# Optimization experiments

Hardware: AMD Instinct MI355X
Metric: run time of the kernel (lower is better)

The kernel has to match this reference:

```python
import jax, jax.numpy as jnp
import numpy as np

T = 10            # inference steps (PCLayer.T)
LOCAL_LR = 0.001  # local_learning_rate
CLAMP = 1.0       # PCLayer.clamp_value


def setup_inputs() -> dict:
    key = jax.random.key(0)
    k1, k2 = jax.random.split(key)
    B, S, H_out, H_in = 8, 1024, 3072, 768
    target_activity = jax.random.normal(k1, (B, S, H_out), dtype=jnp.float32)
    # nn.Linear(H_in, H_out) weight: [H_out, H_in]
    W = jax.random.normal(k2, (H_out, H_in), dtype=jnp.float32) * (1.0 / np.sqrt(H_in))
    b = jnp.zeros((H_out,), dtype=jnp.float32)
    return {"target_activity": target_activity, "W": W, "b": b}


def reference(target_activity, W, b):
    # PCLayer forward, layer_type='fc1' (linear): T-step energy-gradient
    # fixed-point inference on latent x of shape [B, S, H_in].
    B, S, _ = target_activity.shape
    H_in = W.shape[1]
    x0 = jnp.zeros((B, S, H_in), dtype=target_activity.dtype)  # x_init

    def step(x, _):
        mu = jnp.einsum('bsi,oi->bso', x, W) + b       # prediction [B,S,H_out]
        err = target_activity - mu                      # prediction error
        # x <- x - lr * dE/dx, E = 0.5*||err||^2  =>  dE/dx = -err @ W
        x = x + LOCAL_LR * jnp.einsum('bso,oi->bsi', err, W)
        x = jnp.clip(x, -CLAMP, CLAMP)
        return x, None

    x, _ = jax.lax.scan(step, x0, None, length=T)
    return x
```

## Files before the change

kernel.cpp:

```cpp
#include <hip/hip_runtime.h>
#include <stdint.h>


typedef short bf16x8 __attribute__((ext_vector_type(8)));
typedef float f32x4  __attribute__((ext_vector_type(4)));
typedef unsigned short u16;
typedef unsigned int uint_as1 __attribute__((address_space(1)));
typedef unsigned int uint_as3 __attribute__((address_space(3)));

__device__ __forceinline__ u16 f2bf(float f) {
  union { float f; unsigned int i; } x; x.f = f;
  unsigned int r = x.i + 0x7fffu + ((x.i >> 16) & 1u);
  return (u16)(r >> 16);
}
__device__ __forceinline__ void gl2lds16(const void* g, void* l) {
  __builtin_amdgcn_global_load_lds((uint_as1*)(uintptr_t)g,
                                   (uint_as3*)(uintptr_t)l, 16, 0, 0);
}

template<int TM, int NK, int EPI>
__global__ __launch_bounds__(256, 2)
void gemm_lds(const u16* __restrict__ A, const u16* __restrict__ B,
              float* __restrict__ Cf, u16* __restrict__ Cb,
              float alpha, int K, int ldc, int kc, long zstride)
{
  constexpr int FM  = TM / 32;
  constexpr int RPW = TM / 4;
  __shared__ u16 As[TM * 32 * NK];
  __shared__ u16 Bs[128 * 32 * NK];
  const int tid = threadIdx.x, w = tid >> 6, lane = tid & 63;
  const int lm = lane & 15, quad = lane >> 4;
  const int wm = w & 1, wn = w >> 1;
  const int m0 = blockIdx.x * TM, n0 = blockIdx.y * 128;
  const long k0 = (long)blockIdx.z * kc;
  const int r = lane >> 2, q = lane & 3;
  const u16* Ag = A + (long)(m0 + w * RPW + r) * K + k0 + q * 8;
  const u16* Bg = B + (long)(n0 + w * 32 + r) * K + k0 + q * 8;
  u16* Asl = As + w * RPW * 32;
  u16* Bsl = Bs + w * 1024;

  f32x4 acc[FM][4] = {};

  for (int kk = 0; kk < kc; kk += 32 * NK) {
#pragma unroll
    for (int h = 0; h < NK; ++h) {
#pragma unroll
      for (int l = 0; l < RPW / 16; ++l)
        gl2lds16(Ag + (long)(l * 16) * K + kk + h * 32,
                 Asl + h * TM * 32 + l * 512);
      gl2lds16(Bg + kk + h * 32, Bsl + h * 4096);
      gl2lds16(Bg + 16 * (long)K + kk + h * 32, Bsl + h * 4096 + 512);
    }
    __syncthreads();
#pragma unroll
    for (int h = 0; h < NK; ++h) {
      bf16x8 af[FM], bv[4];
#pragma unroll
      for (int i = 0; i < FM; ++i)
        af[i] = *(const bf16x8*)(As + h * TM * 32 +
                                 (wm * (TM / 2) + i * 16 + lm) * 32 + quad * 8);
#pragma unroll
      for (int j = 0; j < 4; ++j)
        bv[j] = *(const bf16x8*)(Bs + h * 4096 +
                                 (wn * 64 + j * 16 + lm) * 32 + quad * 8);
#pragma unroll
      for (int i = 0; i < FM; ++i)
#pragma unroll
        for (int j = 0; j < 4; ++j)
          acc[i][j] = __builtin_amdgcn_mfma_f32_16x16x32_bf16(af[i], bv[j],
                                                              acc[i][j], 0, 0, 0);
    }
    __syncthreads();
  }

  const int rbase = m0 + wm * (TM / 2) + quad * 4;
  const int cbase = n0 + wn * 64 + lm;
  const long zoff = (long)blockIdx.z * zstride;
#pragma unroll
  for (int i = 0; i < FM; ++i)
#pragma unroll
    for (int j = 0; j < 4; ++j) {
      const int col = cbase + j * 16;
#pragma unroll
      for (int rr = 0; rr < 4; ++rr) {
        const long idx = (long)(rbase + i * 16 + rr) * ldc + col;
        const float v = alpha * acc[i][j][rr];
        if constexpr (EPI == 0) Cf[zoff + idx] = v;
        else                    Cb[idx] = f2bf(v);
      }
    }
}

__global__ void conv_all(const float* __restrict__ t, const float* __restrict__ bias,
                         const float* __restrict__ W, u16* __restrict__ tb,
                         u16* __restrict__ Wb, u16* __restrict__ WTb)
{
  const int bx = blockIdx.x, tid = threadIdx.x;
  if (bx < 24576) {
    const long i4 = (long)bx * 256 + tid;
    const float4 v = ((const float4*)t)[i4];
    const float4 bb = ((const float4*)bias)[(int)(i4 % 768)];
    ushort4 o;
    o.x = f2bf(v.x - bb.x); o.y = f2bf(v.y - bb.y);
    o.z = f2bf(v.z - bb.z); o.w = f2bf(v.w - bb.w);
    ((ushort4*)tb)[i4] = o;
  } else {
    const int i4 = (bx - 24576) * 256 + tid;
    const float4 v = ((const float4*)W)[i4];
    ushort4 o;
    o.x = f2bf(v.x); o.y = f2bf(v.y); o.z = f2bf(v.z); o.w = f2bf(v.w);
    ((ushort4*)Wb)[i4] = o;
    const int rr = i4 / 192, c = (i4 - rr * 192) * 4;
    WTb[(long)(c + 0) * 3072 + rr] = o.x;
    WTb[(long)(c + 1) * 3072 + rr] = o.y;
    WTb[(long)(c + 2) * 3072 + rr] = o.z;
    WTb[(long)(c + 3) * 3072 + rr] = o.w;
  }
}

__global__ void red_e(const float* __restrict__ Ep, float* __restrict__ Ef,
                      u16* __restrict__ Eb)
{
  const int i4 = blockIdx.x * 256 + threadIdx.x;
  float4 s = make_float4(0.f, 0.f, 0.f, 0.f);
#pragma unroll
  for (int z = 0; z < 4; ++z) {
    const float4 p = ((const float4*)Ep)[(long)z * 147456 + i4];
    s.x += p.x; s.y += p.y; s.z += p.z; s.w += p.w;
  }
  ((float4*)Ef)[i4] = s;
  ushort4 o; o.x = f2bf(s.x); o.y = f2bf(s.y); o.z = f2bf(s.z); o.w = f2bf(s.w);
  ((ushort4*)Eb)[i4] = o;
}

__global__ void red_m(const float* __restrict__ P2p, const float* __restrict__ Ef,
                      u16* __restrict__ Mb, float lr)
{
  const int i4 = blockIdx.x * 256 + threadIdx.x;
  float4 s = make_float4(0.f, 0.f, 0.f, 0.f);
#pragma unroll
  for (int z = 0; z < 4; ++z) {
    const float4 p = ((const float4*)P2p)[(long)z * 147456 + i4];
    s.x += p.x; s.y += p.y; s.z += p.z; s.w += p.w;
  }
  const float4 e = ((const float4*)Ef)[i4];
  const int rr = i4 / 192, c = (i4 - rr * 192) * 4;
  float4 m;
  m.x = lr * (-45.f * e.x + 120.f * s.x) + (rr == c + 0 ? 0.01f : 0.f);
  m.y = lr * (-45.f * e.y + 120.f * s.y) + (rr == c + 1 ? 0.01f : 0.f);
  m.z = lr * (-45.f * e.z + 120.f * s.z) + (rr == c + 2 ? 0.01f : 0.f);
  m.w = lr * (-45.f * e.w + 120.f * s.w) + (rr == c + 3 ? 0.01f : 0.f);
  ushort4 o; o.x = f2bf(m.x); o.y = f2bf(m.y); o.z = f2bf(m.z); o.w = f2bf(m.w);
  ((ushort4*)Mb)[i4] = o;
}

extern "C" void kernel_launch(void* const* d_in, const int* in_sizes, int n_in,
                              void* d_out, int out_size, void* d_ws, size_t ws_size,
                              hipStream_t stream)
{
  const float* t    = (const float*)d_in[0];
  const float* W    = (const float*)d_in[1];
  const float* bias = (const float*)d_in[2];
  float* out = (float*)d_out;

  char* p = (char*)d_ws;
  u16*   tb  = (u16*)(p + 0);
  u16*   Wb  = (u16*)(p + 50331648);
  u16*   WTb = (u16*)(p + 55050240);
  u16*   Apb = (u16*)(p + 59768832);
  u16*   Eb  = (u16*)(p + 64487424);
  u16*   Mb  = (u16*)(p + 65667072);
  float* Ef  = (float*)(p + 66846720);
  float* R   = (float*)(p + 69206016);
  const float lr = 0.001f;

  conv_all<<<26880, 256, 0, stream>>>(t, bias, W, tb, Wb, WTb);
  gemm_lds<64, 2, 0><<<dim3(12, 6, 4), 256, 0, stream>>>(
      WTb, WTb, R, nullptr, lr, 3072, 768, 768, 589824);
  red_e<<<576, 256, 0, stream>>>(R, Ef, Eb);
  gemm_lds<64, 2, 0><<<dim3(12, 6, 4), 256, 0, stream>>>(
      Eb, Eb, R, nullptr, 1.f, 768, 768, 192, 589824);
  red_m<<<576, 256, 0, stream>>>(R, Ef, Mb, lr);
  gemm_lds<64, 2, 1><<<dim3(12, 24, 1), 256, 0, stream>>>(
      Mb, Wb, nullptr, Apb, 1.f, 768, 3072, 768, 0);
  gemm_lds<128, 2, 0><<<dim3(64, 6, 1), 256, 0, stream>>>(
      tb, Apb, out, nullptr, 1.f, 3072, 768, 3072, 0);
}
```

Before: 276.4 us.

## Reassociate final product through t·W and transpose W via LDS tiles

New measurement: 270.7 us. -2.1%, faster.

```diff
diff --git a/kernel.cpp b/kernel.cpp
--- a/kernel.cpp
+++ b/kernel.cpp
@@ -8,6 +8,9 @@
 typedef unsigned int uint_as1 __attribute__((address_space(1)));
 typedef unsigned int uint_as3 __attribute__((address_space(3)));
 
+__device__ __forceinline__ float bf2f(u16 u) {
+  union { unsigned int i; float f; } x; x.i = ((unsigned int)u) << 16; return x.f;
+}
 __device__ __forceinline__ u16 f2bf(float f) {
   union { float f; unsigned int i; } x; x.f = f;
   unsigned int r = x.i + 0x7fffu + ((x.i >> 16) & 1u);
@@ -22,7 +25,8 @@
 __global__ __launch_bounds__(256, 2)
 void gemm_lds(const u16* __restrict__ A, const u16* __restrict__ B,
               float* __restrict__ Cf, u16* __restrict__ Cb,
-              float alpha, int K, int ldc, int kc, long zstride)
+              const u16* __restrict__ Yb, float alpha, float beta,
+              int K, int ldc, int kc, long zstride)
 {
   constexpr int FM  = TM / 32;
   constexpr int RPW = TM / 4;
@@ -85,16 +89,18 @@
       for (int rr = 0; rr < 4; ++rr) {
         const long idx = (long)(rbase + i * 16 + rr) * ldc + col;
         const float v = alpha * acc[i][j][rr];
-        if constexpr (EPI == 0) Cf[zoff + idx] = v;
-        else                    Cb[idx] = f2bf(v);
+        if constexpr (EPI == 0)      Cf[zoff + idx] = v;
+        else if constexpr (EPI == 1) Cb[idx] = f2bf(v);
+        else                         Cf[idx] = v + beta * bf2f(Yb[idx]);
       }
     }
 }
 
 __global__ void conv_all(const float* __restrict__ t, const float* __restrict__ bias,
                          const float* __restrict__ W, u16* __restrict__ tb,
-                         u16* __restrict__ Wb, u16* __restrict__ WTb)
-{
+                         u16* __restrict__ WTb)
+{
+  __shared__ u16 lds[64 * 72];
   const int bx = blockIdx.x, tid = threadIdx.x;
   if (bx < 24576) {
     const long i4 = (long)bx * 256 + tid;
@@ -105,27 +111,37 @@
     o.z = f2bf(v.z - bb.z); o.w = f2bf(v.w - bb.w);
     ((ushort4*)tb)[i4] = o;
   } else {
-    const int i4 = (bx - 24576) * 256 + tid;
-    const float4 v = ((const float4*)W)[i4];
-    ushort4 o;
-    o.x = f2bf(v.x); o.y = f2bf(v.y); o.z = f2bf(v.z); o.w = f2bf(v.w);
-    ((ushort4*)Wb)[i4] = o;
-    const int rr = i4 / 192, c = (i4 - rr * 192) * 4;
-    WTb[(long)(c + 0) * 3072 + rr] = o.x;
-    WTb[(long)(c + 1) * 3072 + rr] = o.y;
-    WTb[(long)(c + 2) * 3072 + rr] = o.z;
-    WTb[(long)(c + 3) * 3072 + rr] = o.w;
-  }
-}
-
-__global__ void red_e(const float* __restrict__ Ep, float* __restrict__ Ef,
+    const int bt = bx - 24576;
+    const int o0 = (bt / 12) * 64, i0 = (bt % 12) * 64;
+    const int ol = tid >> 2, cg = tid & 3;
+#pragma unroll
+    for (int p = 0; p < 4; ++p) {
+      const float4 v = *(const float4*)(W + (long)(o0 + ol) * 768 + i0 + (cg + p * 4) * 4);
+      const int ib = (cg + p * 4) * 4;
+      lds[(ib + 0) * 72 + ol] = f2bf(v.x);
+      lds[(ib + 1) * 72 + ol] = f2bf(v.y);
+      lds[(ib + 2) * 72 + ol] = f2bf(v.z);
+      lds[(ib + 3) * 72 + ol] = f2bf(v.w);
+    }
+    __syncthreads();
+    const int cl = tid >> 2, og = tid & 3;
+    const u16* src = lds + cl * 72 + og * 16;
+    u16* dst = WTb + (long)(i0 + cl) * 3072 + o0 + og * 16;
+    ((ushort4*)dst)[0] = ((const ushort4*)src)[0];
+    ((ushort4*)dst)[1] = ((const ushort4*)src)[1];
+    ((ushort4*)dst)[2] = ((const ushort4*)src)[2];
+    ((ushort4*)dst)[3] = ((const ushort4*)src)[3];
+  }
+}
+
+__global__ void red_e(const float* __restrict__ R, float* __restrict__ Ef,
                       u16* __restrict__ Eb)
 {
   const int i4 = blockIdx.x * 256 + threadIdx.x;
   float4 s = make_float4(0.f, 0.f, 0.f, 0.f);
 #pragma unroll
-  for (int z = 0; z < 4; ++z) {
-    const float4 p = ((const float4*)Ep)[(long)z * 147456 + i4];
+  for (int z = 0; z < 6; ++z) {
+    const float4 p = ((const float4*)R)[(long)z * 147456 + i4];
     s.x += p.x; s.y += p.y; s.z += p.z; s.w += p.w;
   }
   ((float4*)Ef)[i4] = s;
@@ -133,25 +149,23 @@
   ((ushort4*)Eb)[i4] = o;
 }
 
-__global__ void red_m(const float* __restrict__ P2p, const float* __restrict__ Ef,
-                      u16* __restrict__ Mb, float lr)
+__global__ void red_s(const float* __restrict__ R, const float* __restrict__ Ef,
+                      u16* __restrict__ Spb)
 {
   const int i4 = blockIdx.x * 256 + threadIdx.x;
   float4 s = make_float4(0.f, 0.f, 0.f, 0.f);
 #pragma unroll
-  for (int z = 0; z < 4; ++z) {
-    const float4 p = ((const float4*)P2p)[(long)z * 147456 + i4];
+  for (int z = 0; z < 6; ++z) {
+    const float4 p = ((const float4*)R)[(long)z * 147456 + i4];
     s.x += p.x; s.y += p.y; s.z += p.z; s.w += p.w;
   }
   const float4 e = ((const float4*)Ef)[i4];
-  const int rr = i4 / 192, c = (i4 - rr * 192) * 4;
-  float4 m;
-  m.x = lr * (-45.f * e.x + 120.f * s.x) + (rr == c + 0 ? 0.01f : 0.f);
-  m.y = lr * (-45.f * e.y + 120.f * s.y) + (rr == c + 1 ? 0.01f : 0.f);
-  m.z = lr * (-45.f * e.z + 120.f * s.z) + (rr == c + 2 ? 0.01f : 0.f);
-  m.w = lr * (-45.f * e.w + 120.f * s.w) + (rr == c + 3 ? 0.01f : 0.f);
-  ushort4 o; o.x = f2bf(m.x); o.y = f2bf(m.y); o.z = f2bf(m.z); o.w = f2bf(m.w);
-  ((ushort4*)Mb)[i4] = o;
+  ushort4 o;
+  o.x = f2bf(-45.f * e.x + 120.f * s.x);
+  o.y = f2bf(-45.f * e.y + 120.f * s.y);
+  o.z = f2bf(-45.f * e.z + 120.f * s.z);
+  o.w = f2bf(-45.f * e.w + 120.f * s.w);
+  ((ushort4*)Spb)[i4] = o;
 }
 
 extern "C" void kernel_launch(void* const* d_in, const int* in_sizes, int n_in,
@@ -165,24 +179,23 @@
 
   char* p = (char*)d_ws;
   u16*   tb  = (u16*)(p + 0);
-  u16*   Wb  = (u16*)(p + 50331648);
-  u16*   WTb = (u16*)(p + 55050240);
-  u16*   Apb = (u16*)(p + 59768832);
-  u16*   Eb  = (u16*)(p + 64487424);
-  u16*   Mb  = (u16*)(p + 65667072);
-  float* Ef  = (float*)(p + 66846720);
-  float* R   = (float*)(p + 69206016);
+  u16*   WTb = (u16*)(p + 50331648);
+  float* Ef  = (float*)(p + 55050240);
+  u16*   Eb  = (u16*)(p + 57409536);
+  u16*   Spb = (u16*)(p + 58589184);
+  float* R   = (float*)(p + 59768832);
+  u16*   yb  = (u16*)(p + 59768832);
   const float lr = 0.001f;
 
-  conv_all<<<26880, 256, 0, stream>>>(t, bias, W, tb, Wb, WTb);
-  gemm_lds<64, 2, 0><<<dim3(12, 6, 4), 256, 0, stream>>>(
-      WTb, WTb, R, nullptr, lr, 3072, 768, 768, 589824);
+  conv_all<<<25152, 256, 0, stream>>>(t, bias, W, tb, WTb);
+  gemm_lds<64, 2, 0><<<dim3(12, 6, 6), 256, 0, stream>>>(
+      WTb, WTb, R, nullptr, nullptr, lr, 0.f, 3072, 768, 512, 589824);
   red_e<<<576, 256, 0, stream>>>(R, Ef, Eb);
-  gemm_lds<64, 2, 0><<<dim3(12, 6, 4), 256, 0, stream>>>(
-      Eb, Eb, R, nullptr, 1.f, 768, 768, 192, 589824);
-  red_m<<<576, 256, 0, stream>>>(R, Ef, Mb, lr);
-  gemm_lds<64, 2, 1><<<dim3(12, 24, 1), 256, 0, stream>>>(
-      Mb, Wb, nullptr, Apb, 1.f, 768, 3072, 768, 0);
-  gemm_lds<128, 2, 0><<<dim3(64, 6, 1), 256, 0, stream>>>(
-      tb, Apb, out, nullptr, 1.f, 3072, 768, 3072, 0);
-}
+  gemm_lds<64, 2, 0><<<dim3(12, 6, 6), 256, 0, stream>>>(
+      Eb, Eb, R, nullptr, nullptr, 1.f, 0.f, 768, 768, 128, 589824);
+  red_s<<<576, 256, 0, stream>>>(R, Ef, Spb);
+  gemm_lds<128, 2, 1><<<dim3(64, 6, 1), 256, 0, stream>>>(
+      tb, WTb, nullptr, yb, nullptr, 1.f, 0.f, 3072, 768, 3072, 0);
+  gemm_lds<128, 2, 2><<<dim3(64, 6, 1), 256, 0, stream>>>(
+      yb, Spb, out, nullptr, yb, lr, 0.01f, 768, 768, 768, 0);
+}
```
